# Optimization experiments

Measured on AMD Instinct MI355X. Metric: run time of the kernel, lower is better.

The kernel has to match this reference:

```python
import jax, jax.numpy as jnp
import numpy as np

N = 6144          # number_of_nodes
E = 196608        # random edges (self-loops appended in reference, as add_self_loops does)
L_GAT = 10        # GAT num_layers
NEG_SLOPE = 0.2   # GATConv leaky_relu slope


def setup_inputs() -> dict:
    key = jax.random.key(0)
    ks = jax.random.split(key, 27)
    g = lambda i, shape, s=0.3: jax.random.normal(ks[i], shape, jnp.float32) * s
    return {
        "x": jax.random.normal(ks[0], (N, 3), jnp.float32),
        "mask": jax.random.uniform(ks[1], (N,), dtype=jnp.float32),
        "edge_index": jax.random.randint(ks[2], (2, E), 0, N),
        # 10-layer GAT (heads=1): per-layer lin weight, att_src, att_dst, bias
        "gat_W": g(3, (L_GAT, 3, 3)), "gat_asrc": g(4, (L_GAT, 3)),
        "gat_adst": g(5, (L_GAT, 3)), "gat_b": g(6, (L_GAT, 3), 0.1),
        # nn.MultiheadAttention(embed_dim=3, num_heads=3)
        "mha_in_w": g(7, (9, 3)), "mha_in_b": g(8, (9,), 0.1),
        "mha_out_w": g(9, (3, 3)), "mha_out_b": g(10, (3,), 0.1),
        # TransformerConv(3, 3, heads=1)
        "tc_Wq": g(11, (3, 3)), "tc_bq": g(12, (3,), 0.1),
        "tc_Wk": g(13, (3, 3)), "tc_bk": g(14, (3,), 0.1),
        "tc_Wv": g(15, (3, 3)), "tc_bv": g(16, (3,), 0.1),
        "tc_Wskip": g(17, (3, 3)), "tc_bskip": g(18, (3,), 0.1),
        # actor MLP: Linear(3N,16) -> ReLU -> Linear(16,32) -> ReLU -> Linear(32,N)
        "mlp_W1": g(19, (3 * N, 16), 0.02), "mlp_b1": g(20, (16,), 0.1),
        "mlp_W2": g(21, (16, 32), 0.2), "mlp_b2": g(22, (32,), 0.1),
        "mlp_W3": g(23, (32, N), 0.2), "mlp_b3": jnp.zeros((N,), jnp.float32),
        # critic Linear(1,1)
        "critic_W": g(24, (1, 1)), "critic_b": g(25, (1,), 0.1),
    }


def _seg_softmax(e, seg, n):
    # numerically-stable softmax grouped by destination node
    m = jax.lax.stop_gradient(jax.ops.segment_max(e, seg, num_segments=n))
    w = jnp.exp(e - m[seg])
    z = jax.ops.segment_sum(w, seg, num_segments=n)
    return w / (z[seg] + 1e-16)


def reference(x, mask, edge_index, gat_W, gat_asrc, gat_adst, gat_b,
              mha_in_w, mha_in_b, mha_out_w, mha_out_b,
              tc_Wq, tc_bq, tc_Wk, tc_bk, tc_Wv, tc_bv, tc_Wskip, tc_bskip,
              mlp_W1, mlp_b1, mlp_W2, mlp_b2, mlp_W3, mlp_b3,
              critic_W, critic_b):
    n = x.shape[0]
    loops = jnp.arange(n)
    src = jnp.concatenate([edge_index[0], loops])  # add_self_loops
    dst = jnp.concatenate([edge_index[1], loops])

    # ---- 10-layer GAT (heads=1, ReLU between layers) ----
    h = x
    for l in range(L_GAT):
        xp = h @ gat_W[l]                                   # [N,3]
        e = jax.nn.leaky_relu(xp[src] @ gat_asrc[l] + xp[dst] @ gat_adst[l], NEG_SLOPE)
        alpha = _seg_softmax(e, dst, n)
        h_new = jax.ops.segment_sum(alpha[:, None] * xp[src], dst, num_segments=n) + gat_b[l]
        h = jax.nn.relu(h_new) if l < L_GAT - 1 else h_new

    # ---- MultiheadAttention(embed_dim=3, num_heads=3 => head_dim=1), history = [h] ----
    qkv = h @ mha_in_w.T + mha_in_b                         # [N,9]
    q, k, v = qkv[:, 0:3], qkv[:, 3:6], qkv[:, 6:9]
    scores = jnp.einsum('nh,mh->hnm', q, k)                 # head_dim=1 -> scale = 1
    attn = jax.nn.softmax(scores, axis=-1)                  # [3,N,N] -- dominant memory
    o = jnp.einsum('hnm,mh->nh', attn, v)                   # [N,3]
    h2 = o @ mha_out_w.T + mha_out_b

    # ---- TransformerConv(3, 3, heads=1) ----
    q2 = h2 @ tc_Wq + tc_bq
    k2 = h2 @ tc_Wk + tc_bk
    v2 = h2 @ tc_Wv + tc_bv
    logit = (q2[dst] * k2[src]).sum(-1) * (1.0 / np.sqrt(3.0))
    alpha2 = _seg_softmax(logit, dst, n)
    agg = jax.ops.segment_sum(alpha2[:, None] * v2[src], dst, num_segments=n)
    h3 = agg + h2 @ tc_Wskip + tc_bskip                     # root_weight skip

    # ---- actor MLP over flattened node features ----
    flat = h3.reshape(-1)                                   # [3N]
    a1 = jax.nn.relu(flat @ mlp_W1 + mlp_b1)
    a2 = jax.nn.relu(a1 @ mlp_W2 + mlp_b2)
    results = (a2 @ mlp_W3 + mlp_b3)[:, None]               # [N,1]

    new_results = results[:, 0] * mask
    value = jnp.mean(results @ critic_W + critic_b)
    return new_results, value
```

## Files before the change

### kernel.cpp

```cpp
#include <hip/hip_runtime.h>

#define N 6144
#define E 196608
#define EN (E + N)
#define LGAT 10
#define LOG2E 1.4426950408889634f

typedef unsigned int u32;

__device__ __forceinline__ u32 f2key(float f) {
    u32 u = __float_as_uint(f);
    return (u & 0x80000000u) ? ~u : (u | 0x80000000u);
}
__device__ __forceinline__ float key2f(u32 k) {
    u32 u = (k & 0x80000000u) ? (k & 0x7FFFFFFFu) : ~k;
    return __uint_as_float(u);
}

struct P {
    const float *x, *mask, *gat_W, *gat_asrc, *gat_adst, *gat_b;
    const float *in_w, *in_b, *out_w, *out_b;
    const float *Wq, *bq, *Wk, *bk, *Wv, *bv, *Wsk, *bsk;
    const float *W1, *b1, *W2, *b2, *W3, *b3, *cW, *cb;
    const int *src, *dst;
    float4 *nodeA, *nodeB;
    float *sdstA, *sdstB;
    float *q3, *q2, *h2, *h3, *part;
    float4 *kvpack4;
    float4 *kv2;
    float *a1pre, *a2buf, *sumres;
    u32 *deg, *offs, *cursor, *kmaxk, *kmink;
    int *ssorted;
    float *out;
};

__global__ void k_hist(P p) {
    int e = blockIdx.x * 256 + threadIdx.x;
    if (e < N) {
        float h0 = p.x[e * 3 + 0], h1 = p.x[e * 3 + 1], h2 = p.x[e * 3 + 2];
        const float* W = p.gat_W;
        float xp0 = h0 * W[0] + h1 * W[3] + h2 * W[6];
        float xp1 = h0 * W[1] + h1 * W[4] + h2 * W[7];
        float xp2 = h0 * W[2] + h1 * W[5] + h2 * W[8];
        float ss = LOG2E * (xp0 * p.gat_asrc[0] + xp1 * p.gat_asrc[1] + xp2 * p.gat_asrc[2]);
        p.nodeA[e] = make_float4(xp0, xp1, xp2, ss);
        p.sdstA[e] = LOG2E * (xp0 * p.gat_adst[0] + xp1 * p.gat_adst[1] + xp2 * p.gat_adst[2]);
    }
    if (e >= EN) return;
    int d = (e < E) ? p.dst[e] : (e - E);
    atomicAdd(&p.deg[d], 1u);
}

__global__ void k_scan(P p) {
    __shared__ u32 part[256];
    int t = threadIdx.x;
    if (t < 3) p.kmaxk[t] = 0u;
    else if (t < 6) p.kmink[t - 3] = 0xFFFFFFFFu;
    else if (t < 22) p.a1pre[t - 6] = 0.f;
    else if (t == 22) p.sumres[0] = 0.f;
    u32 loc[24];
    u32 sum = 0;
    #pragma unroll
    for (int i = 0; i < 24; ++i) { loc[i] = sum; sum += p.deg[t * 24 + i]; }
    part[t] = sum;
    __syncthreads();
    for (int o = 1; o < 256; o <<= 1) {
        u32 v = (t >= o) ? part[t - o] : 0u;
        __syncthreads();
        part[t] += v;
        __syncthreads();
    }
    u32 base = (t == 0) ? 0u : part[t - 1];
    #pragma unroll
    for (int i = 0; i < 24; ++i) {
        u32 off = base + loc[i];
        p.offs[t * 24 + i] = off;
        p.cursor[t * 24 + i] = off;
    }
    if (t == 255) p.offs[N] = part[255];
}

__global__ void k_scatter(P p) {
    int e = blockIdx.x * 256 + threadIdx.x;
    if (e >= EN) return;
    int s = (e < E) ? p.src[e] : (e - E);
    int d = (e < E) ? p.dst[e] : (e - E);
    u32 pos = atomicAdd(&p.cursor[d], 1u);
    p.ssorted[pos] = s;
}

__global__ void k_gat_edge(P p, const float4* __restrict__ nin,
                           const float* __restrict__ sdin,
                           float4* __restrict__ nout, float* __restrict__ sdout,
                           int l) {
    int gid = blockIdx.x * 256 + threadIdx.x;
    int d = gid >> 5;
    int lane = gid & 31;
    u32 beg = p.offs[d], end = p.offs[d + 1];
    float sd = sdin[d];
    u32 i0 = beg + lane, i1 = i0 + 32, i2 = i0 + 64, i3 = i0 + 96;
    bool e0 = i0 < end, e1 = i1 < end, e2 = i2 < end, e3 = i3 < end;
    int j0 = e0 ? p.ssorted[i0] : 0;
    int j1 = e1 ? p.ssorted[i1] : 0;
    int j2 = e2 ? p.ssorted[i2] : 0;
    int j3 = e3 ? p.ssorted[i3] : 0;
    float4 r0 = nin[j0], r1 = nin[j1], r2 = nin[j2], r3 = nin[j3];
    float v0 = r0.w + sd; v0 = (v0 >= 0.f) ? v0 : 0.2f * v0; v0 = e0 ? v0 : -1e30f;
    float v1 = r1.w + sd; v1 = (v1 >= 0.f) ? v1 : 0.2f * v1; v1 = e1 ? v1 : -1e30f;
    float v2 = r2.w + sd; v2 = (v2 >= 0.f) ? v2 : 0.2f * v2; v2 = e2 ? v2 : -1e30f;
    float v3 = r3.w + sd; v3 = (v3 >= 0.f) ? v3 : 0.2f * v3; v3 = e3 ? v3 : -1e30f;
    float mx = fmaxf(fmaxf(v0, v1), fmaxf(v2, v3));
    for (u32 i = i0 + 128; i < end; i += 32) {
        float4 r = nin[p.ssorted[i]];
        float v = r.w + sd; v = (v >= 0.f) ? v : 0.2f * v;
        mx = fmaxf(mx, v);
    }
    #pragma unroll
    for (int o = 1; o < 32; o <<= 1) mx = fmaxf(mx, __shfl_xor(mx, o));
    float w0 = exp2f(v0 - mx), w1 = exp2f(v1 - mx),
          w2 = exp2f(v2 - mx), w3 = exp2f(v3 - mx);
    float sz = w0 + w1 + w2 + w3;
    float s0 = w0 * r0.x + w1 * r1.x + w2 * r2.x + w3 * r3.x;
    float s1 = w0 * r0.y + w1 * r1.y + w2 * r2.y + w3 * r3.y;
    float s2 = w0 * r0.z + w1 * r1.z + w2 * r2.z + w3 * r3.z;
    for (u32 i = i0 + 128; i < end; i += 32) {
        float4 r = nin[p.ssorted[i]];
        float v = r.w + sd; v = (v >= 0.f) ? v : 0.2f * v;
        float w = exp2f(v - mx);
        sz += w; s0 += w * r.x; s1 += w * r.y; s2 += w * r.z;
    }
    #pragma unroll
    for (int o = 1; o < 32; o <<= 1) {
        sz += __shfl_xor(sz, o);
        s0 += __shfl_xor(s0, o);
        s1 += __shfl_xor(s1, o);
        s2 += __shfl_xor(s2, o);
    }
    if (lane == 0) {
        float z = sz + 1e-16f;
        float o0 = s0 / z + p.gat_b[l * 3 + 0];
        float o1 = s1 / z + p.gat_b[l * 3 + 1];
        float o2 = s2 / z + p.gat_b[l * 3 + 2];
        if (l < LGAT - 1) {
            o0 = fmaxf(o0, 0.f); o1 = fmaxf(o1, 0.f); o2 = fmaxf(o2, 0.f);
            const float* W = p.gat_W + (l + 1) * 9;
            float xp0 = o0 * W[0] + o1 * W[3] + o2 * W[6];
            float xp1 = o0 * W[1] + o1 * W[4] + o2 * W[7];
            float xp2 = o0 * W[2] + o1 * W[5] + o2 * W[8];
            const float* as = p.gat_asrc + (l + 1) * 3;
            const float* ad = p.gat_adst + (l + 1) * 3;
            float ss = LOG2E * (xp0 * as[0] + xp1 * as[1] + xp2 * as[2]);
            nout[d] = make_float4(xp0, xp1, xp2, ss);
            sdout[d] = LOG2E * (xp0 * ad[0] + xp1 * ad[1] + xp2 * ad[2]);
        } else {
            float pr[9];
            #pragma unroll
            for (int j = 0; j < 9; ++j)
                pr[j] = o0 * p.in_w[j * 3 + 0] + o1 * p.in_w[j * 3 + 1] +
                        o2 * p.in_w[j * 3 + 2] + p.in_b[j];
            p.q3[d * 3 + 0] = pr[0]; p.q3[d * 3 + 1] = pr[1]; p.q3[d * 3 + 2] = pr[2];
            p.kvpack4[d * 2 + 0] = make_float4(pr[3], pr[4], pr[5], pr[6]);
            p.kvpack4[d * 2 + 1] = make_float4(pr[7], pr[8], 0.f, 0.f);
        }
    }
}

__global__ void k_kminmax(P p) {
    int n = blockIdx.x * 256 + threadIdx.x;
    float4 a = p.kvpack4[n * 2];
    float kk[3] = {a.x, a.y, a.z};
    #pragma unroll
    for (int hh = 0; hh < 3; ++hh) {
        float mx = kk[hh], mn = kk[hh];
        #pragma unroll
        for (int o = 32; o; o >>= 1) {
            mx = fmaxf(mx, __shfl_xor(mx, o));
            mn = fminf(mn, __shfl_xor(mn, o));
        }
        if ((threadIdx.x & 63) == 0) {
            atomicMax(&p.kmaxk[hh], f2key(mx));
            atomicMin(&p.kmink[hh], f2key(mn));
        }
    }
}

#define MCH 192
__global__ void k_att_partial(P p) {
    __shared__ float4 kv4[MCH * 2];
    int tid = threadIdx.x;
    int chunk = blockIdx.y;
    int mbase = chunk * MCH;
    for (int i = tid; i < MCH * 2; i += 256) kv4[i] = p.kvpack4[mbase * 2 + i];
    __syncthreads();
    int n = blockIdx.x * 256 + tid;
    float q0 = p.q3[n * 3 + 0], q1 = p.q3[n * 3 + 1], q2 = p.q3[n * 3 + 2];
    float kmx0 = key2f(p.kmaxk[0]), kmx1 = key2f(p.kmaxk[1]), kmx2 = key2f(p.kmaxk[2]);
    float kmn0 = key2f(p.kmink[0]), kmn1 = key2f(p.kmink[1]), kmn2 = key2f(p.kmink[2]);
    float q0s = q0 * LOG2E, q1s = q1 * LOG2E, q2s = q2 * LOG2E;
    float nM0 = -((q0 >= 0.f) ? q0s * kmx0 : q0s * kmn0);
    float nM1 = -((q1 >= 0.f) ? q1s * kmx1 : q1s * kmn1);
    float nM2 = -((q2 >= 0.f) ? q2s * kmx2 : q2s * kmn2);
    float num0 = 0, den0 = 0, num1 = 0, den1 = 0, num2 = 0, den2 = 0;
    #pragma unroll 4
    for (int mm = 0; mm < MCH; ++mm) {
        float4 a = kv4[mm * 2], b = kv4[mm * 2 + 1];
        float t0 = exp2f(fmaf(q0s, a.x, nM0)); den0 += t0; num0 = fmaf(t0, a.w, num0);
        float t1 = exp2f(fmaf(q1s, a.y, nM1)); den1 += t1; num1 = fmaf(t1, b.x, num1);
        float t2 = exp2f(fmaf(q2s, a.z, nM2)); den2 += t2; num2 = fmaf(t2, b.y, num2);
    }
    float* pp = p.part + (size_t)chunk * 6 * N + n;
    pp[0] = num0; pp[N] = den0; pp[2 * N] = num1;
    pp[3 * N] = den1; pp[4 * N] = num2; pp[5 * N] = den2;
}

__global__ void k_att_reduce(P p) {
    int n = blockIdx.x * 256 + threadIdx.x;
    float num[3] = {0.f, 0.f, 0.f}, den[3] = {0.f, 0.f, 0.f};
    for (int c = 0; c < 32; ++c) {
        const float* pp = p.part + (size_t)c * 6 * N + n;
        #pragma unroll
        for (int hh = 0; hh < 3; ++hh) {
            num[hh] += pp[hh * 2 * N];
            den[hh] += pp[(hh * 2 + 1) * N];
        }
    }
    float o[3];
    #pragma unroll
    for (int hh = 0; hh < 3; ++hh) o[hh] = num[hh] / den[hh];
    float h2v[3];
    #pragma unroll
    for (int c = 0; c < 3; ++c) {
        h2v[c] = p.out_b[c] + o[0] * p.out_w[c * 3 + 0] +
                 o[1] * p.out_w[c * 3 + 1] + o[2] * p.out_w[c * 3 + 2];
        p.h2[n * 3 + c] = h2v[c];
    }
    float q2v[3], k2v[3], v2v[3];
    #pragma unroll
    for (int c = 0; c < 3; ++c) {
        q2v[c] = p.bq[c] + h2v[0] * p.Wq[c] + h2v[1] * p.Wq[3 + c] + h2v[2] * p.Wq[6 + c];
        k2v[c] = p.bk[c] + h2v[0] * p.Wk[c] + h2v[1] * p.Wk[3 + c] + h2v[2] * p.Wk[6 + c];
        v2v[c] = p.bv[c] + h2v[0] * p.Wv[c] + h2v[1] * p.Wv[3 + c] + h2v[2] * p.Wv[6 + c];
        p.q2[n * 3 + c] = q2v[c];
    }
    p.kv2[n * 2 + 0] = make_float4(k2v[0], k2v[1], k2v[2], v2v[0]);
    p.kv2[n * 2 + 1] = make_float4(v2v[1], v2v[2], 0.f, 0.f);
}

__global__ void k_tc_edge(P p) {
    int gid = blockIdx.x * 256 + threadIdx.x;
    int d = gid >> 5;
    int lane = gid & 31;
    u32 beg = p.offs[d], end = p.offs[d + 1];
    float q0 = p.q2[d * 3 + 0], q1 = p.q2[d * 3 + 1], q2 = p.q2[d * 3 + 2];
    const float RS3L = 0.57735026919f * LOG2E;
    u32 i0 = beg + lane, i1 = i0 + 32;
    bool e0 = i0 < end, e1 = i1 < end;
    int j0 = e0 ? p.ssorted[i0] : 0;
    int j1 = e1 ? p.ssorted[i1] : 0;
    float4 ka0 = p.kv2[j0 * 2], kb0 = p.kv2[j0 * 2 + 1];
    float4 ka1 = p.kv2[j1 * 2], kb1 = p.kv2[j1 * 2 + 1];
    float g0 = (q0 * ka0.x + q1 * ka0.y + q2 * ka0.z) * RS3L; g0 = e0 ? g0 : -1e30f;
    float g1 = (q0 * ka1.x + q1 * ka1.y + q2 * ka1.z) * RS3L; g1 = e1 ? g1 : -1e30f;
    float mx = fmaxf(g0, g1);
    for (u32 i = i0 + 64; i < end; i += 32) {
        float4 ka = p.kv2[p.ssorted[i] * 2];
        mx = fmaxf(mx, (q0 * ka.x + q1 * ka.y + q2 * ka.z) * RS3L);
    }
    #pragma unroll
    for (int o = 1; o < 32; o <<= 1) mx = fmaxf(mx, __shfl_xor(mx, o));
    float w0 = exp2f(g0 - mx), w1 = exp2f(g1 - mx);
    float sz = w0 + w1;
    float s0 = w0 * ka0.w + w1 * ka1.w;
    float s1 = w0 * kb0.x + w1 * kb1.x;
    float s2 = w0 * kb0.y + w1 * kb1.y;
    for (u32 i = i0 + 64; i < end; i += 32) {
        int s = p.ssorted[i];
        float4 ka = p.kv2[s * 2], kb = p.kv2[s * 2 + 1];
        float g = (q0 * ka.x + q1 * ka.y + q2 * ka.z) * RS3L;
        float w = exp2f(g - mx);
        sz += w; s0 += w * ka.w; s1 += w * kb.x; s2 += w * kb.y;
    }
    #pragma unroll
    for (int o = 1; o < 32; o <<= 1) {
        sz += __shfl_xor(sz, o);
        s0 += __shfl_xor(s0, o);
        s1 += __shfl_xor(s1, o);
        s2 += __shfl_xor(s2, o);
    }
    if (lane == 0) {
        float z = sz + 1e-16f;
        float h0 = p.h2[d * 3 + 0], h1 = p.h2[d * 3 + 1], h2 = p.h2[d * 3 + 2];
        float agg[3] = {s0 / z, s1 / z, s2 / z};
        #pragma unroll
        for (int c = 0; c < 3; ++c) {
            p.h3[d * 3 + c] = agg[c] + p.bsk[c] +
                h0 * p.Wsk[c] + h1 * p.Wsk[3 + c] + h2 * p.Wsk[6 + c];
        }
    }
}

__global__ void k_mlp1(P p) {
    __shared__ float red[64];
    int t = blockIdx.x * 256 + threadIdx.x;
    int j = t & 15;
    int g = t >> 4;
    float acc = 0.f;
    #pragma unroll
    for (int k = 0; k < 16; ++k) {
        int r = g + k * 1152;
        acc += p.h3[r] * p.W1[r * 16 + j];
    }
    acc += __shfl_xor(acc, 16);
    acc += __shfl_xor(acc, 32);
    int tid = threadIdx.x;
    if ((tid & 63) < 16) red[(tid >> 6) * 16 + j] = acc;
    __syncthreads();
    if (tid < 16) {
        float s = red[tid] + red[16 + tid] + red[32 + tid] + red[48 + tid];
        atomicAdd(&p.a1pre[tid], s);
    }
}

__global__ void k_mlp2(P p) {
    __shared__ float a1[16];
    int t = threadIdx.x;
    if (t < 16) a1[t] = fmaxf(p.a1pre[t] + p.b1[t], 0.f);
    __syncthreads();
    if (t < 32) {
        float acc = p.b2[t];
        #pragma unroll
        for (int i = 0; i < 16; ++i) acc += a1[i] * p.W2[i * 32 + t];
        p.a2buf[t] = fmaxf(acc, 0.f);
    }
}

__global__ void k_mlp3(P p) {
    __shared__ float a2[32];
    if (threadIdx.x < 32) a2[threadIdx.x] = p.a2buf[threadIdx.x];
    __syncthreads();
    int n = blockIdx.x * 256 + threadIdx.x;
    float acc = p.b3[n];
    #pragma unroll
    for (int j = 0; j < 32; ++j) acc += a2[j] * p.W3[(size_t)j * N + n];
    p.out[n] = acc * p.mask[n];
    float s = acc;
    #pragma unroll
    for (int o = 32; o; o >>= 1) s += __shfl_xor(s, o);
    if ((threadIdx.x & 63) == 0) atomicAdd(p.sumres, s);
}

__global__ void k_value(P p) {
    p.out[N] = p.cW[0] * (p.sumres[0] / (float)N) + p.cb[0];
}

extern "C" void kernel_launch(void* const* d_in, const int* in_sizes, int n_in,
                              void* d_out, int out_size, void* d_ws, size_t ws_size,
                              hipStream_t stream) {
    P p;
    p.x      = (const float*)d_in[0];
    p.mask   = (const float*)d_in[1];
    const int* ei = (const int*)d_in[2];
    p.src = ei; p.dst = ei + E;
    p.gat_W  = (const float*)d_in[3];
    p.gat_asrc = (const float*)d_in[4];
    p.gat_adst = (const float*)d_in[5];
    p.gat_b  = (const float*)d_in[6];
    p.in_w   = (const float*)d_in[7];
    p.in_b   = (const float*)d_in[8];
    p.out_w  = (const float*)d_in[9];
    p.out_b  = (const float*)d_in[10];
    p.Wq = (const float*)d_in[11]; p.bq = (const float*)d_in[12];
    p.Wk = (const float*)d_in[13]; p.bk = (const float*)d_in[14];
    p.Wv = (const float*)d_in[15]; p.bv = (const float*)d_in[16];
    p.Wsk = (const float*)d_in[17]; p.bsk = (const float*)d_in[18];
    p.W1 = (const float*)d_in[19]; p.b1 = (const float*)d_in[20];
    p.W2 = (const float*)d_in[21]; p.b2 = (const float*)d_in[22];
    p.W3 = (const float*)d_in[23]; p.b3 = (const float*)d_in[24];
    p.cW = (const float*)d_in[25]; p.cb = (const float*)d_in[26];

    float* ws = (float*)d_ws;
    p.nodeA   = (float4*)(ws + 0);
    p.nodeB   = (float4*)(ws + 24576);
    p.sdstA   = ws + 49152;
    p.sdstB   = ws + 55296;
    p.q3      = ws + 61440;
    p.kvpack4 = (float4*)(ws + 79872);
    p.q2      = ws + 129024;
    p.kv2     = (float4*)(ws + 147456);
    p.h2      = ws + 196608;
    p.h3      = ws + 215040;
    p.part    = ws + 233472;
    p.a1pre   = ws + 1413120;
    p.a2buf   = ws + 1413136;
    p.sumres  = ws + 1413168;
    p.kmaxk   = (u32*)(ws + 1413172);
    p.kmink   = (u32*)(ws + 1413175);
    p.deg     = (u32*)(ws + 1413178);
    p.offs    = (u32*)(ws + 1419322);
    p.cursor  = (u32*)(ws + 1425467);
    p.ssorted = (int*)(ws + 1431611);
    p.out     = (float*)d_out;

    hipMemsetAsync(p.deg, 0, N * sizeof(u32), stream);
    k_hist<<<792, 256, 0, stream>>>(p);
    k_scan<<<1, 256, 0, stream>>>(p);
    k_scatter<<<792, 256, 0, stream>>>(p);
    for (int l = 0; l < LGAT; ++l) {
        const float4* nin = (l & 1) ? p.nodeB : p.nodeA;
        const float*  sdin = (l & 1) ? p.sdstB : p.sdstA;
        float4* nout = (l & 1) ? p.nodeA : p.nodeB;
        float*  sdout = (l & 1) ? p.sdstA : p.sdstB;
        k_gat_edge<<<768, 256, 0, stream>>>(p, nin, sdin, nout, sdout, l);
    }
    k_kminmax<<<24, 256, 0, stream>>>(p);
    k_att_partial<<<dim3(24, 32), 256, 0, stream>>>(p);
    k_att_reduce<<<24, 256, 0, stream>>>(p);
    k_tc_edge<<<768, 256, 0, stream>>>(p);
    k_mlp1<<<72, 256, 0, stream>>>(p);
    k_mlp2<<<1, 64, 0, stream>>>(p);
    k_mlp3<<<24, 256, 0, stream>>>(p);
    k_value<<<1, 1, 0, stream>>>(p);
}
```

Baseline: 254.2 us.

## Fuse whole pipeline into one cooperative persistent kernel with grid syncs

Replaces the sequence of about twenty kernel launches (histogram, scan, scatter, ten GAT layers, attention, TransformerConv, MLP, value) with a single cooperative kernel that runs each stage as a grid-stride phase separated by grid.sync(). The aim is to remove per-launch overhead and inter-kernel gaps, which are large relative to the small per-stage work. In exchange, each grid-wide barrier has its own cost, the grid is limited to co-resident blocks (launch bounds 256,2), and serial phases like the scan and mlp2 now leave the rest of the grid idle at a barrier. The multi-kernel path is kept as a fallback when cooperative launch is unavailable.

```diff
diff --git a/kernel.cpp b/kernel.cpp
--- a/kernel.cpp
+++ b/kernel.cpp
@@ -1,10 +1,14 @@
 #include <hip/hip_runtime.h>
+#include <hip/hip_cooperative_groups.h>
+
+namespace cg = cooperative_groups;
 
 #define N 6144
 #define E 196608
 #define EN (E + N)
 #define LGAT 10
 #define LOG2E 1.4426950408889634f
+#define MCH 192
 
 typedef unsigned int u32;
 
@@ -33,6 +37,339 @@
     int *ssorted;
     float *out;
 };
+
+__global__ void __launch_bounds__(256, 2) k_mega(P p) {
+    cg::grid_group grid = cg::this_grid();
+    const int b = blockIdx.x;
+    const int tid = threadIdx.x;
+    const int gid = b * 256 + tid;
+    const int NB = gridDim.x;
+    const int NT = NB * 256;
+    const int NG = NT >> 5;
+    const int lane = gid & 31;
+    const int g0 = gid >> 5;
+
+    __shared__ u32 spart[256];
+    __shared__ float4 kv4[MCH * 2];
+    __shared__ float red[64];
+    __shared__ float a1s[16];
+    __shared__ float a2s[32];
+
+    for (int t = gid; t < N; t += NT) p.deg[t] = 0u;
+    if (gid < 3) p.kmaxk[gid] = 0u;
+    else if (gid < 6) p.kmink[gid - 3] = 0xFFFFFFFFu;
+    else if (gid < 22) p.a1pre[gid - 6] = 0.f;
+    else if (gid == 22) p.sumres[0] = 0.f;
+    grid.sync();
+
+    for (int n = gid; n < N; n += NT) {
+        float h0 = p.x[n * 3 + 0], h1 = p.x[n * 3 + 1], h2 = p.x[n * 3 + 2];
+        const float* W = p.gat_W;
+        float xp0 = h0 * W[0] + h1 * W[3] + h2 * W[6];
+        float xp1 = h0 * W[1] + h1 * W[4] + h2 * W[7];
+        float xp2 = h0 * W[2] + h1 * W[5] + h2 * W[8];
+        float ss = LOG2E * (xp0 * p.gat_asrc[0] + xp1 * p.gat_asrc[1] + xp2 * p.gat_asrc[2]);
+        p.nodeA[n] = make_float4(xp0, xp1, xp2, ss);
+        p.sdstA[n] = LOG2E * (xp0 * p.gat_adst[0] + xp1 * p.gat_adst[1] + xp2 * p.gat_adst[2]);
+    }
+    for (int e = gid; e < EN; e += NT) {
+        int d = (e < E) ? p.dst[e] : (e - E);
+        atomicAdd(&p.deg[d], 1u);
+    }
+    grid.sync();
+
+    if (b == 0) {
+        int t = tid;
+        u32 loc[24];
+        u32 sum = 0;
+        #pragma unroll
+        for (int i = 0; i < 24; ++i) { loc[i] = sum; sum += p.deg[t * 24 + i]; }
+        spart[t] = sum;
+        __syncthreads();
+        for (int o = 1; o < 256; o <<= 1) {
+            u32 v = (t >= o) ? spart[t - o] : 0u;
+            __syncthreads();
+            spart[t] += v;
+            __syncthreads();
+        }
+        u32 base = (t == 0) ? 0u : spart[t - 1];
+        #pragma unroll
+        for (int i = 0; i < 24; ++i) {
+            u32 off = base + loc[i];
+            p.offs[t * 24 + i] = off;
+            p.cursor[t * 24 + i] = off;
+        }
+        if (t == 255) p.offs[N] = spart[255];
+    }
+    grid.sync();
+
+    for (int e = gid; e < EN; e += NT) {
+        int s = (e < E) ? p.src[e] : (e - E);
+        int d = (e < E) ? p.dst[e] : (e - E);
+        u32 pos = atomicAdd(&p.cursor[d], 1u);
+        p.ssorted[pos] = s;
+    }
+    grid.sync();
+
+    float4* nin = p.nodeA;  float* sdin = p.sdstA;
+    float4* nout = p.nodeB; float* sdout = p.sdstB;
+    for (int l = 0; l < LGAT; ++l) {
+        for (int d = g0; d < N; d += NG) {
+            u32 beg = p.offs[d], end = p.offs[d + 1];
+            float sd = sdin[d];
+            u32 i0 = beg + lane, i1 = i0 + 32, i2 = i0 + 64, i3 = i0 + 96;
+            bool e0 = i0 < end, e1 = i1 < end, e2 = i2 < end, e3 = i3 < end;
+            int j0 = e0 ? p.ssorted[i0] : 0;
+            int j1 = e1 ? p.ssorted[i1] : 0;
+            int j2 = e2 ? p.ssorted[i2] : 0;
+            int j3 = e3 ? p.ssorted[i3] : 0;
+            float4 r0 = nin[j0], r1 = nin[j1], r2 = nin[j2], r3 = nin[j3];
+            float v0 = r0.w + sd; v0 = (v0 >= 0.f) ? v0 : 0.2f * v0; v0 = e0 ? v0 : -1e30f;
+            float v1 = r1.w + sd; v1 = (v1 >= 0.f) ? v1 : 0.2f * v1; v1 = e1 ? v1 : -1e30f;
+            float v2 = r2.w + sd; v2 = (v2 >= 0.f) ? v2 : 0.2f * v2; v2 = e2 ? v2 : -1e30f;
+            float v3 = r3.w + sd; v3 = (v3 >= 0.f) ? v3 : 0.2f * v3; v3 = e3 ? v3 : -1e30f;
+            float mx = fmaxf(fmaxf(v0, v1), fmaxf(v2, v3));
+            for (u32 i = i0 + 128; i < end; i += 32) {
+                float4 r = nin[p.ssorted[i]];
+                float v = r.w + sd; v = (v >= 0.f) ? v : 0.2f * v;
+                mx = fmaxf(mx, v);
+            }
+            #pragma unroll
+            for (int o = 1; o < 32; o <<= 1) mx = fmaxf(mx, __shfl_xor(mx, o));
+            float w0 = exp2f(v0 - mx), w1 = exp2f(v1 - mx),
+                  w2 = exp2f(v2 - mx), w3 = exp2f(v3 - mx);
+            float sz = w0 + w1 + w2 + w3;
+            float s0 = w0 * r0.x + w1 * r1.x + w2 * r2.x + w3 * r3.x;
+            float s1 = w0 * r0.y + w1 * r1.y + w2 * r2.y + w3 * r3.y;
+            float s2 = w0 * r0.z + w1 * r1.z + w2 * r2.z + w3 * r3.z;
+            for (u32 i = i0 + 128; i < end; i += 32) {
+                float4 r = nin[p.ssorted[i]];
+                float v = r.w + sd; v = (v >= 0.f) ? v : 0.2f * v;
+                float w = exp2f(v - mx);
+                sz += w; s0 += w * r.x; s1 += w * r.y; s2 += w * r.z;
+            }
+            #pragma unroll
+            for (int o = 1; o < 32; o <<= 1) {
+                sz += __shfl_xor(sz, o);
+                s0 += __shfl_xor(s0, o);
+                s1 += __shfl_xor(s1, o);
+                s2 += __shfl_xor(s2, o);
+            }
+            if (lane == 0) {
+                float z = sz + 1e-16f;
+                float o0 = s0 / z + p.gat_b[l * 3 + 0];
+                float o1 = s1 / z + p.gat_b[l * 3 + 1];
+                float o2 = s2 / z + p.gat_b[l * 3 + 2];
+                if (l < LGAT - 1) {
+                    o0 = fmaxf(o0, 0.f); o1 = fmaxf(o1, 0.f); o2 = fmaxf(o2, 0.f);
+                    const float* W = p.gat_W + (l + 1) * 9;
+                    float xp0 = o0 * W[0] + o1 * W[3] + o2 * W[6];
+                    float xp1 = o0 * W[1] + o1 * W[4] + o2 * W[7];
+                    float xp2 = o0 * W[2] + o1 * W[5] + o2 * W[8];
+                    const float* as = p.gat_asrc + (l + 1) * 3;
+                    const float* ad = p.gat_adst + (l + 1) * 3;
+                    float ss = LOG2E * (xp0 * as[0] + xp1 * as[1] + xp2 * as[2]);
+                    nout[d] = make_float4(xp0, xp1, xp2, ss);
+                    sdout[d] = LOG2E * (xp0 * ad[0] + xp1 * ad[1] + xp2 * ad[2]);
+                } else {
+                    float pr[9];
+                    #pragma unroll
+                    for (int j = 0; j < 9; ++j)
+                        pr[j] = o0 * p.in_w[j * 3 + 0] + o1 * p.in_w[j * 3 + 1] +
+                                o2 * p.in_w[j * 3 + 2] + p.in_b[j];
+                    p.q3[d * 3 + 0] = pr[0]; p.q3[d * 3 + 1] = pr[1]; p.q3[d * 3 + 2] = pr[2];
+                    p.kvpack4[d * 2 + 0] = make_float4(pr[3], pr[4], pr[5], pr[6]);
+                    p.kvpack4[d * 2 + 1] = make_float4(pr[7], pr[8], 0.f, 0.f);
+                }
+            }
+        }
+        grid.sync();
+        float4* tn = nin; nin = nout; nout = tn;
+        float* ts = sdin; sdin = sdout; sdout = ts;
+    }
+
+    if (gid < N) {
+        float4 a = p.kvpack4[gid * 2];
+        float kk[3] = {a.x, a.y, a.z};
+        #pragma unroll
+        for (int hh = 0; hh < 3; ++hh) {
+            float mx = kk[hh], mn = kk[hh];
+            #pragma unroll
+            for (int o = 32; o; o >>= 1) {
+                mx = fmaxf(mx, __shfl_xor(mx, o));
+                mn = fminf(mn, __shfl_xor(mn, o));
+            }
+            if ((tid & 63) == 0) {
+                atomicMax(&p.kmaxk[hh], f2key(mx));
+                atomicMin(&p.kmink[hh], f2key(mn));
+            }
+        }
+    }
+    grid.sync();
+
+    for (int vb = b; vb < 768; vb += NB) {
+        int chunk = vb & 31;
+        int ntile = vb >> 5;
+        __syncthreads();
+        for (int i = tid; i < MCH * 2; i += 256) kv4[i] = p.kvpack4[chunk * MCH * 2 + i];
+        __syncthreads();
+        int n = ntile * 256 + tid;
+        float q0 = p.q3[n * 3 + 0], q1 = p.q3[n * 3 + 1], q2 = p.q3[n * 3 + 2];
+        float kmx0 = key2f(p.kmaxk[0]), kmx1 = key2f(p.kmaxk[1]), kmx2 = key2f(p.kmaxk[2]);
+        float kmn0 = key2f(p.kmink[0]), kmn1 = key2f(p.kmink[1]), kmn2 = key2f(p.kmink[2]);
+        float q0s = q0 * LOG2E, q1s = q1 * LOG2E, q2s = q2 * LOG2E;
+        float nM0 = -((q0 >= 0.f) ? q0s * kmx0 : q0s * kmn0);
+        float nM1 = -((q1 >= 0.f) ? q1s * kmx1 : q1s * kmn1);
+        float nM2 = -((q2 >= 0.f) ? q2s * kmx2 : q2s * kmn2);
+        float num0 = 0, den0 = 0, num1 = 0, den1 = 0, num2 = 0, den2 = 0;
+        #pragma unroll 2
+        for (int mm = 0; mm < MCH; ++mm) {
+            float4 a = kv4[mm * 2], bb = kv4[mm * 2 + 1];
+            float t0 = exp2f(fmaf(q0s, a.x, nM0)); den0 += t0; num0 = fmaf(t0, a.w, num0);
+            float t1 = exp2f(fmaf(q1s, a.y, nM1)); den1 += t1; num1 = fmaf(t1, bb.x, num1);
+            float t2 = exp2f(fmaf(q2s, a.z, nM2)); den2 += t2; num2 = fmaf(t2, bb.y, num2);
+        }
+        float* pp = p.part + (size_t)chunk * 6 * N + n;
+        pp[0] = num0; pp[N] = den0; pp[2 * N] = num1;
+        pp[3 * N] = den1; pp[4 * N] = num2; pp[5 * N] = den2;
+    }
+    grid.sync();
+
+    if (gid < N) {
+        int n = gid;
+        float num[3] = {0.f, 0.f, 0.f}, den[3] = {0.f, 0.f, 0.f};
+        for (int c = 0; c < 32; ++c) {
+            const float* pp = p.part + (size_t)c * 6 * N + n;
+            #pragma unroll
+            for (int hh = 0; hh < 3; ++hh) {
+                num[hh] += pp[hh * 2 * N];
+                den[hh] += pp[(hh * 2 + 1) * N];
+            }
+        }
+        float o[3];
+        #pragma unroll
+        for (int hh = 0; hh < 3; ++hh) o[hh] = num[hh] / den[hh];
+        float h2v[3];
+        #pragma unroll
+        for (int c = 0; c < 3; ++c) {
+            h2v[c] = p.out_b[c] + o[0] * p.out_w[c * 3 + 0] +
+                     o[1] * p.out_w[c * 3 + 1] + o[2] * p.out_w[c * 3 + 2];
+            p.h2[n * 3 + c] = h2v[c];
+        }
+        float q2v[3], k2v[3], v2v[3];
+        #pragma unroll
+        for (int c = 0; c < 3; ++c) {
+            q2v[c] = p.bq[c] + h2v[0] * p.Wq[c] + h2v[1] * p.Wq[3 + c] + h2v[2] * p.Wq[6 + c];
+            k2v[c] = p.bk[c] + h2v[0] * p.Wk[c] + h2v[1] * p.Wk[3 + c] + h2v[2] * p.Wk[6 + c];
+            v2v[c] = p.bv[c] + h2v[0] * p.Wv[c] + h2v[1] * p.Wv[3 + c] + h2v[2] * p.Wv[6 + c];
+            p.q2[n * 3 + c] = q2v[c];
+        }
+        p.kv2[n * 2 + 0] = make_float4(k2v[0], k2v[1], k2v[2], v2v[0]);
+        p.kv2[n * 2 + 1] = make_float4(v2v[1], v2v[2], 0.f, 0.f);
+    }
+    grid.sync();
+
+    for (int d = g0; d < N; d += NG) {
+        u32 beg = p.offs[d], end = p.offs[d + 1];
+        float q0 = p.q2[d * 3 + 0], q1 = p.q2[d * 3 + 1], q2 = p.q2[d * 3 + 2];
+        const float RS3L = 0.57735026919f * LOG2E;
+        u32 i0 = beg + lane, i1 = i0 + 32;
+        bool e0 = i0 < end, e1 = i1 < end;
+        int j0 = e0 ? p.ssorted[i0] : 0;
+        int j1 = e1 ? p.ssorted[i1] : 0;
+        float4 ka0 = p.kv2[j0 * 2], kb0 = p.kv2[j0 * 2 + 1];
+        float4 ka1 = p.kv2[j1 * 2], kb1 = p.kv2[j1 * 2 + 1];
+        float gg0 = (q0 * ka0.x + q1 * ka0.y + q2 * ka0.z) * RS3L; gg0 = e0 ? gg0 : -1e30f;
+        float gg1 = (q0 * ka1.x + q1 * ka1.y + q2 * ka1.z) * RS3L; gg1 = e1 ? gg1 : -1e30f;
+        float mx = fmaxf(gg0, gg1);
+        for (u32 i = i0 + 64; i < end; i += 32) {
+            float4 ka = p.kv2[p.ssorted[i] * 2];
+            mx = fmaxf(mx, (q0 * ka.x + q1 * ka.y + q2 * ka.z) * RS3L);
+        }
+        #pragma unroll
+        for (int o = 1; o < 32; o <<= 1) mx = fmaxf(mx, __shfl_xor(mx, o));
+        float w0 = exp2f(gg0 - mx), w1 = exp2f(gg1 - mx);
+        float sz = w0 + w1;
+        float s0 = w0 * ka0.w + w1 * ka1.w;
+        float s1 = w0 * kb0.x + w1 * kb1.x;
+        float s2 = w0 * kb0.y + w1 * kb1.y;
+        for (u32 i = i0 + 64; i < end; i += 32) {
+            int s = p.ssorted[i];
+            float4 ka = p.kv2[s * 2], kb = p.kv2[s * 2 + 1];
+            float g = (q0 * ka.x + q1 * ka.y + q2 * ka.z) * RS3L;
+            float w = exp2f(g - mx);
+            sz += w; s0 += w * ka.w; s1 += w * kb.x; s2 += w * kb.y;
+        }
+        #pragma unroll
+        for (int o = 1; o < 32; o <<= 1) {
+            sz += __shfl_xor(sz, o);
+            s0 += __shfl_xor(s0, o);
+            s1 += __shfl_xor(s1, o);
+            s2 += __shfl_xor(s2, o);
+        }
+        if (lane == 0) {
+            float z = sz + 1e-16f;
+            float h0 = p.h2[d * 3 + 0], h1 = p.h2[d * 3 + 1], h2 = p.h2[d * 3 + 2];
+            float agg[3] = {s0 / z, s1 / z, s2 / z};
+            #pragma unroll
+            for (int c = 0; c < 3; ++c) {
+                p.h3[d * 3 + c] = agg[c] + p.bsk[c] +
+                    h0 * p.Wsk[c] + h1 * p.Wsk[3 + c] + h2 * p.Wsk[6 + c];
+            }
+        }
+    }
+    grid.sync();
+
+    if (b < 72) {
+        int t = gid;
+        int j = t & 15;
+        int g = t >> 4;
+        float acc = 0.f;
+        #pragma unroll
+        for (int k = 0; k < 16; ++k) {
+            int r = g + k * 1152;
+            acc += p.h3[r] * p.W1[r * 16 + j];
+        }
+        acc += __shfl_xor(acc, 16);
+        acc += __shfl_xor(acc, 32);
+        if ((tid & 63) < 16) red[(tid >> 6) * 16 + j] = acc;
+        __syncthreads();
+        if (tid < 16) {
+            float s = red[tid] + red[16 + tid] + red[32 + tid] + red[48 + tid];
+            atomicAdd(&p.a1pre[tid], s);
+        }
+    }
+    grid.sync();
+
+    if (b == 0) {
+        if (tid < 16) a1s[tid] = fmaxf(p.a1pre[tid] + p.b1[tid], 0.f);
+        __syncthreads();
+        if (tid < 32) {
+            float acc = p.b2[tid];
+            #pragma unroll
+            for (int i = 0; i < 16; ++i) acc += a1s[i] * p.W2[i * 32 + tid];
+            p.a2buf[tid] = fmaxf(acc, 0.f);
+        }
+    }
+    grid.sync();
+
+    if (b < 24) {
+        if (tid < 32) a2s[tid] = p.a2buf[tid];
+        __syncthreads();
+        int n = gid;
+        float acc = p.b3[n];
+        #pragma unroll
+        for (int j = 0; j < 32; ++j) acc += a2s[j] * p.W3[(size_t)j * N + n];
+        p.out[n] = acc * p.mask[n];
+        float s = acc;
+        #pragma unroll
+        for (int o = 32; o; o >>= 1) s += __shfl_xor(s, o);
+        if ((tid & 63) == 0) atomicAdd(p.sumres, s);
+    }
+    grid.sync();
+
+    if (gid == 0) p.out[N] = p.cW[0] * (p.sumres[0] / (float)N) + p.cb[0];
+}
 
 __global__ void k_hist(P p) {
     int e = blockIdx.x * 256 + threadIdx.x;
@@ -184,13 +521,11 @@
     }
 }
 
-#define MCH 192
 __global__ void k_att_partial(P p) {
     __shared__ float4 kv4[MCH * 2];
     int tid = threadIdx.x;
     int chunk = blockIdx.y;
-    int mbase = chunk * MCH;
-    for (int i = tid; i < MCH * 2; i += 256) kv4[i] = p.kvpack4[mbase * 2 + i];
+    for (int i = tid; i < MCH * 2; i += 256) kv4[i] = p.kvpack4[chunk * MCH * 2 + i];
     __syncthreads();
     int n = blockIdx.x * 256 + tid;
     float q0 = p.q3[n * 3 + 0], q1 = p.q3[n * 3 + 1], q2 = p.q3[n * 3 + 2];
@@ -201,12 +536,12 @@
     float nM1 = -((q1 >= 0.f) ? q1s * kmx1 : q1s * kmn1);
     float nM2 = -((q2 >= 0.f) ? q2s * kmx2 : q2s * kmn2);
     float num0 = 0, den0 = 0, num1 = 0, den1 = 0, num2 = 0, den2 = 0;
-    #pragma unroll 4
+    #pragma unroll 2
     for (int mm = 0; mm < MCH; ++mm) {
-        float4 a = kv4[mm * 2], b = kv4[mm * 2 + 1];
+        float4 a = kv4[mm * 2], bb = kv4[mm * 2 + 1];
         float t0 = exp2f(fmaf(q0s, a.x, nM0)); den0 += t0; num0 = fmaf(t0, a.w, num0);
-        float t1 = exp2f(fmaf(q1s, a.y, nM1)); den1 += t1; num1 = fmaf(t1, b.x, num1);
-        float t2 = exp2f(fmaf(q2s, a.z, nM2)); den2 += t2; num2 = fmaf(t2, b.y, num2);
+        float t1 = exp2f(fmaf(q1s, a.y, nM1)); den1 += t1; num1 = fmaf(t1, bb.x, num1);
+        float t2 = exp2f(fmaf(q2s, a.z, nM2)); den2 += t2; num2 = fmaf(t2, bb.y, num2);
     }
     float* pp = p.part + (size_t)chunk * 6 * N + n;
     pp[0] = num0; pp[N] = den0; pp[2 * N] = num1;
@@ -401,23 +736,39 @@
     p.ssorted = (int*)(ws + 1431611);
     p.out     = (float*)d_out;
 
-    hipMemsetAsync(p.deg, 0, N * sizeof(u32), stream);
-    k_hist<<<792, 256, 0, stream>>>(p);
-    k_scan<<<1, 256, 0, stream>>>(p);
-    k_scatter<<<792, 256, 0, stream>>>(p);
-    for (int l = 0; l < LGAT; ++l) {
-        const float4* nin = (l & 1) ? p.nodeB : p.nodeA;
-        const float*  sdin = (l & 1) ? p.sdstB : p.sdstA;
-        float4* nout = (l & 1) ? p.nodeA : p.nodeB;
-        float*  sdout = (l & 1) ? p.sdstA : p.sdstB;
-        k_gat_edge<<<768, 256, 0, stream>>>(p, nin, sdin, nout, sdout, l);
-    }
-    k_kminmax<<<24, 256, 0, stream>>>(p);
-    k_att_partial<<<dim3(24, 32), 256, 0, stream>>>(p);
-    k_att_reduce<<<24, 256, 0, stream>>>(p);
-    k_tc_edge<<<768, 256, 0, stream>>>(p);
-    k_mlp1<<<72, 256, 0, stream>>>(p);
-    k_mlp2<<<1, 64, 0, stream>>>(p);
-    k_mlp3<<<24, 256, 0, stream>>>(p);
-    k_value<<<1, 1, 0, stream>>>(p);
-}
+    int coopOK = 0, numCU = 0, maxPerCU = 0;
+    hipDeviceGetAttribute(&coopOK, hipDeviceAttributeCooperativeLaunch, 0);
+    hipDeviceGetAttribute(&numCU, hipDeviceAttributeMultiprocessorCount, 0);
+    hipOccupancyMaxActiveBlocksPerMultiprocessor(&maxPerCU, k_mega, 256, 0);
+    int nb = maxPerCU * numCU;
+    if (nb > 768) nb = 768;
+
+    bool done = false;
+    if (coopOK && nb >= 72) {
+        void* args[] = { (void*)&p };
+        if (hipLaunchCooperativeKernel((const void*)k_mega, dim3(nb), dim3(256),
+                                       args, 0, stream) == hipSuccess)
+            done = true;
+    }
+    if (!done) {
+        hipMemsetAsync(p.deg, 0, N * sizeof(u32), stream);
+        k_hist<<<792, 256, 0, stream>>>(p);
+        k_scan<<<1, 256, 0, stream>>>(p);
+        k_scatter<<<792, 256, 0, stream>>>(p);
+        for (int l = 0; l < LGAT; ++l) {
+            const float4* nin = (l & 1) ? p.nodeB : p.nodeA;
+            const float*  sdin = (l & 1) ? p.sdstB : p.sdstA;
+            float4* nout = (l & 1) ? p.nodeA : p.nodeB;
+            float*  sdout = (l & 1) ? p.sdstA : p.sdstB;
+            k_gat_edge<<<768, 256, 0, stream>>>(p, nin, sdin, nout, sdout, l);
+        }
+        k_kminmax<<<24, 256, 0, stream>>>(p);
+        k_att_partial<<<dim3(24, 32), 256, 0, stream>>>(p);
+        k_att_reduce<<<24, 256, 0, stream>>>(p);
+        k_tc_edge<<<768, 256, 0, stream>>>(p);
+        k_mlp1<<<72, 256, 0, stream>>>(p);
+        k_mlp2<<<1, 64, 0, stream>>>(p);
+        k_mlp3<<<24, 256, 0, stream>>>(p);
+        k_value<<<1, 1, 0, stream>>>(p);
+    }
+}
```

New measurement: 861.5 us. 239% more time.
